# Optimization experiments

Measured on AMD Instinct MI355X. Metric: run time of the kernel, lower is better.

## Reference

```python
import jax, jax.numpy as jnp
import numpy as np

V, D, M, C, L = 100000, 256, 4096, 4096, 32
PAD = 0
EPS = 1e-8  # torch CosineSimilarity default eps


def setup_inputs() -> dict:
    key = jax.random.key(0)
    ks = jax.random.split(key, 6)
    xs = jax.random.randint(ks[0], (1, L), 0, V)
    mems = jax.random.randint(ks[1], (M, L), 0, V)
    ys = jax.random.randint(ks[2], (1, L), 0, V)
    cands = jax.random.randint(ks[3], (C, L), 0, V)
    lt = jax.random.normal(ks[4], (V, D), dtype=jnp.float32) * 0.02
    lt = lt.at[PAD].set(0.0)  # nn.Embedding padding_idx row is zero
    freqs = jax.random.uniform(ks[5], (V,), dtype=jnp.float32, minval=0.05, maxval=1.0)
    return {"xs": xs, "mems": mems, "ys": ys, "cands": cands, "lt": lt, "freqs": freqs}


def _encode(tokens, lt, freqs):
    # Batched Encoder.forward: freq-weighted average of token embeddings.
    # tokens: [N, L] -> [N, D]
    emb = lt[tokens]                       # [N, L, D] gather
    w = freqs[tokens]                      # [N, L]
    w = w / jnp.linalg.norm(w, axis=1, keepdims=True)  # w * (1 / ||w||)
    return jnp.einsum('nl,nld->nd', w, emb)


def reference(xs, mems, ys, cands, lt, freqs):
    xs_emb = _encode(xs, lt, freqs)                                   # [1, D]
    mems_enc = jnp.concatenate([_encode(mems, lt, freqs), xs_emb], 0)  # [M+1, D]
    # cosine similarity of xs_emb (broadcast) against each memory row
    an = jnp.maximum(jnp.linalg.norm(xs_emb, axis=1), EPS)            # [1]
    bn = jnp.maximum(jnp.linalg.norm(mems_enc, axis=1), EPS)          # [M+1]
    cos = (mems_enc @ xs_emb[0]) / (an * bn)                          # [M+1]
    att = jax.nn.softmax(cos)[None, :]                                # [1, M+1]
    lhs_emb = att @ mems_enc                                          # [1, D]
    ys_emb = _encode(ys, lt, freqs)                                   # [1, D]
    cand_emb = _encode(cands, lt, freqs)                              # [C, D]
    # torch.cat of lhs_emb repeated (1 + C) times; ys then cand encodings
    xs_out = jnp.tile(lhs_emb, (cands.shape[0] + 1, 1))               # [C+1, D]
    ys_out = jnp.concatenate([ys_emb, cand_emb], axis=0)              # [C+1, D]
    return xs_out, ys_out
```

## Files before the change

kernel.cpp:

```cpp
#include <hip/hip_runtime.h>

#define V_ 100000
#define D_ 256
#define M_ 4096
#define C_ 4096
#define L_ 32
#define ROWS_MEMS (M_ + 1)
#define NTASK (1 + M_ + 1 + C_)

__device__ __forceinline__ float wave_allreduce_sum(float v) {
    #pragma unroll
    for (int off = 32; off >= 1; off >>= 1) v += __shfl_xor(v, off, 64);
    return v;
}

__device__ __forceinline__ float lane_bcast_f(float v, int l) {
    return __uint_as_float((unsigned)__builtin_amdgcn_readlane((int)__float_as_uint(v), l));
}

__device__ __forceinline__ float4 encode_row(const int* __restrict__ tok_ptr,
                                             const char* __restrict__ ltb,
                                             const float* __restrict__ freqs,
                                             const int lane, const unsigned voff) {
    int tok = 0; float w = 0.f;
    if (lane < L_) { tok = tok_ptr[lane]; w = freqs[tok]; }
    const float s2 = wave_allreduce_sum(w * w);
    const float wn = w / sqrtf(s2);

    float4 acc = make_float4(0.f, 0.f, 0.f, 0.f);
    #pragma unroll
    for (int lb = 0; lb < L_; lb += 8) {
        float4 v[8];
        #pragma unroll
        for (int j = 0; j < 8; ++j) {
            const unsigned t = (unsigned)__builtin_amdgcn_readlane(tok, lb + j);
            v[j] = *reinterpret_cast<const float4*>(
                ltb + t * (unsigned)(D_ * sizeof(float)) + voff);
        }
        #pragma unroll
        for (int j = 0; j < 8; ++j) {
            const float wl = lane_bcast_f(wn, lb + j);
            acc.x = fmaf(wl, v[j].x, acc.x);
            acc.y = fmaf(wl, v[j].y, acc.y);
            acc.z = fmaf(wl, v[j].z, acc.z);
            acc.w = fmaf(wl, v[j].w, acc.w);
        }
    }
    return acc;
}

__global__ __launch_bounds__(256) void encode_fused(
    const int* __restrict__ xs, const int* __restrict__ mems,
    const int* __restrict__ ys, const int* __restrict__ cands,
    const float* __restrict__ lt, const float* __restrict__ freqs,
    float* __restrict__ lhs_raw,
    float* __restrict__ gsum,
    float* __restrict__ out_ys)
{
    __shared__ float s_xf[D_];
    __shared__ float s_an2;
    __shared__ float s_lred[D_];
    __shared__ float s_ered;

    const int wave = threadIdx.x >> 6;
    const int lane = threadIdx.x & 63;
    const int d0 = lane * 4;
    const unsigned voff = (unsigned)d0 * sizeof(float);
    const char* ltb = (const char*)lt;
    const int rt0 = blockIdx.x * 4;
    const bool block_has_att = (rt0 <= M_);

    s_lred[threadIdx.x] = 0.f;
    if (threadIdx.x == 0) s_ered = 0.f;

    if (block_has_att && wave == 0) {
        const float4 xf = encode_row(xs, ltb, freqs, lane, voff);
        *reinterpret_cast<float4*>(&s_xf[d0]) = xf;
        const float an2 = wave_allreduce_sum(xf.x*xf.x + xf.y*xf.y + xf.z*xf.z + xf.w*xf.w);
        if (lane == 0) s_an2 = an2;
    }
    __syncthreads();

    const int rt = rt0 + wave;
    if (rt < NTASK) {
        const int* tok_ptr; float* dst = nullptr; bool has_att = false;
        if (rt == 0) {
            tok_ptr = xs; has_att = true;
        } else if (rt <= M_) {
            tok_ptr = mems + (size_t)(rt - 1) * L_; has_att = true;
        } else if (rt == M_ + 1) {
            tok_ptr = ys; dst = out_ys;
        } else {
            const int c = rt - (M_ + 2);
            tok_ptr = cands + (size_t)c * L_;
            dst = out_ys + (size_t)(c + 1) * D_;
        }

        const float4 acc = encode_row(tok_ptr, ltb, freqs, lane, voff);

        if (has_att) {
            const float4 xf = *reinterpret_cast<const float4*>(&s_xf[d0]);
            const float d = wave_allreduce_sum(acc.x*xf.x + acc.y*xf.y + acc.z*xf.z + acc.w*xf.w);
            const float q = wave_allreduce_sum(acc.x*acc.x + acc.y*acc.y + acc.z*acc.z + acc.w*acc.w);
            const float an = fmaxf(sqrtf(s_an2), 1e-8f);
            const float bn = fmaxf(sqrtf(q),  1e-8f);
            const float e = expf(d / (an * bn));
            atomicAdd(&s_lred[d0 + 0], e * acc.x);
            atomicAdd(&s_lred[d0 + 1], e * acc.y);
            atomicAdd(&s_lred[d0 + 2], e * acc.z);
            atomicAdd(&s_lred[d0 + 3], e * acc.w);
            if (lane == 0) atomicAdd(&s_ered, e);
        } else {
            *reinterpret_cast<float4*>(dst + d0) = acc;
        }
    }

    if (block_has_att) {
        __syncthreads();
        atomicAdd(&lhs_raw[threadIdx.x], s_lred[threadIdx.x]);
        if (threadIdx.x == 0) atomicAdd(gsum, s_ered);
    }
}

__global__ __launch_bounds__(256) void finalize_tile(
    const float* __restrict__ lhs_raw, const float* __restrict__ gsum,
    float* __restrict__ out_xs)
{
    const float val = lhs_raw[threadIdx.x] / gsum[0];
    for (int r = blockIdx.x; r < ROWS_MEMS; r += gridDim.x)
        out_xs[(size_t)r * D_ + threadIdx.x] = val;
}

extern "C" void kernel_launch(void* const* d_in, const int* in_sizes, int n_in,
                              void* d_out, int out_size, void* d_ws, size_t ws_size,
                              hipStream_t stream) {
    const int*   xs    = (const int*)d_in[0];
    const int*   mems  = (const int*)d_in[1];
    const int*   ys    = (const int*)d_in[2];
    const int*   cands = (const int*)d_in[3];
    const float* lt    = (const float*)d_in[4];
    const float* freqs = (const float*)d_in[5];

    float* out    = (float*)d_out;
    float* out_xs = out;
    float* out_ys = out + (size_t)ROWS_MEMS * D_;

    float* lhs_raw = (float*)d_ws;
    float* gsum    = lhs_raw + D_;

    hipMemsetAsync(lhs_raw, 0, (D_ + 1) * sizeof(float), stream);

    encode_fused<<<(NTASK + 3) / 4, 256, 0, stream>>>(xs, mems, ys, cands, lt, freqs,
                                                      lhs_raw, gsum, out_ys);
    finalize_tile<<<1024, 256, 0, stream>>>(lhs_raw, gsum, out_xs);
}
```

Before: 192.1 us.

## Precompute xs encoding in separate kernel and spread atomics over partial buffers

Adds a one-block pre-kernel that encodes xs once and zeroes a set of 32 partial-sum buffers, replacing the memset. Each attention block then loads the precomputed xs vector instead of re-encoding it with a wave. The global atomic accumulation is spread across 32 buffers by block index to reduce contention, and the finalize kernel sums those partials. This costs an extra kernel launch and more reads in finalize.

```diff
diff --git a/kernel.cpp b/kernel.cpp
--- a/kernel.cpp
+++ b/kernel.cpp
@@ -7,6 +7,9 @@
 #define L_ 32
 #define ROWS_MEMS (M_ + 1)
 #define NTASK (1 + M_ + 1 + C_)
+
+#define NBUF 32
+#define BSTRIDE 260
 
 __device__ __forceinline__ float wave_allreduce_sum(float v) {
     #pragma unroll
@@ -18,10 +21,10 @@
     return __uint_as_float((unsigned)__builtin_amdgcn_readlane((int)__float_as_uint(v), l));
 }
 
-__device__ __forceinline__ float4 encode_row(const int* __restrict__ tok_ptr,
-                                             const char* __restrict__ ltb,
-                                             const float* __restrict__ freqs,
-                                             const int lane, const unsigned voff) {
+__device__ __forceinline__ float4 encode_row_f(const int* __restrict__ tok_ptr,
+                                               const char* __restrict__ ltb,
+                                               const float* __restrict__ freqs,
+                                               const int lane, const unsigned voff) {
     int tok = 0; float w = 0.f;
     if (lane < L_) { tok = tok_ptr[lane]; w = freqs[tok]; }
     const float s2 = wave_allreduce_sum(w * w);
@@ -34,8 +37,7 @@
         #pragma unroll
         for (int j = 0; j < 8; ++j) {
             const unsigned t = (unsigned)__builtin_amdgcn_readlane(tok, lb + j);
-            v[j] = *reinterpret_cast<const float4*>(
-                ltb + t * (unsigned)(D_ * sizeof(float)) + voff);
+            v[j] = *reinterpret_cast<const float4*>(ltb + t * 1024u + voff);
         }
         #pragma unroll
         for (int j = 0; j < 8; ++j) {
@@ -49,35 +51,51 @@
     return acc;
 }
 
+__global__ __launch_bounds__(256) void xs_pre(
+    const int* __restrict__ xs, const float* __restrict__ lt,
+    const float* __restrict__ freqs, float* __restrict__ part,
+    float* __restrict__ g_xs)
+{
+    for (int i = threadIdx.x; i < NBUF * BSTRIDE; i += 256) part[i] = 0.f;
+
+    if (threadIdx.x < 64) {
+        const int lane = threadIdx.x;
+        const unsigned voff = (unsigned)lane * 16u;
+        const float4 acc = encode_row_f(xs, (const char*)lt, freqs, lane, voff);
+        *reinterpret_cast<float4*>(g_xs + lane * 4) = acc;
+        const float an2 = wave_allreduce_sum(acc.x*acc.x + acc.y*acc.y +
+                                             acc.z*acc.z + acc.w*acc.w);
+        if (lane == 0) g_xs[256] = an2;
+    }
+}
+
 __global__ __launch_bounds__(256) void encode_fused(
     const int* __restrict__ xs, const int* __restrict__ mems,
     const int* __restrict__ ys, const int* __restrict__ cands,
     const float* __restrict__ lt, const float* __restrict__ freqs,
-    float* __restrict__ lhs_raw,
-    float* __restrict__ gsum,
+    const float* __restrict__ g_xs,
+    float* __restrict__ part,
     float* __restrict__ out_ys)
 {
     __shared__ float s_xf[D_];
-    __shared__ float s_an2;
     __shared__ float s_lred[D_];
     __shared__ float s_ered;
+    __shared__ float s_an2;
 
-    const int wave = threadIdx.x >> 6;
-    const int lane = threadIdx.x & 63;
+    const int tid  = threadIdx.x;
+    const int wave = tid >> 6;
+    const int lane = tid & 63;
     const int d0 = lane * 4;
-    const unsigned voff = (unsigned)d0 * sizeof(float);
+    const unsigned voff = (unsigned)d0 * 4u;
     const char* ltb = (const char*)lt;
     const int rt0 = blockIdx.x * 4;
     const bool block_has_att = (rt0 <= M_);
 
-    s_lred[threadIdx.x] = 0.f;
-    if (threadIdx.x == 0) s_ered = 0.f;
-
-    if (block_has_att && wave == 0) {
-        const float4 xf = encode_row(xs, ltb, freqs, lane, voff);
-        *reinterpret_cast<float4*>(&s_xf[d0]) = xf;
-        const float an2 = wave_allreduce_sum(xf.x*xf.x + xf.y*xf.y + xf.z*xf.z + xf.w*xf.w);
-        if (lane == 0) s_an2 = an2;
+    s_lred[tid] = 0.f;
+    if (tid == 0) s_ered = 0.f;
+    if (block_has_att) {
+        s_xf[tid] = g_xs[tid];
+        if (tid == 0) s_an2 = g_xs[256];
     }
     __syncthreads();
 
@@ -96,7 +114,7 @@
             dst = out_ys + (size_t)(c + 1) * D_;
         }
 
-        const float4 acc = encode_row(tok_ptr, ltb, freqs, lane, voff);
+        const float4 acc = encode_row_f(tok_ptr, ltb, freqs, lane, voff);
 
         if (has_att) {
             const float4 xf = *reinterpret_cast<const float4*>(&s_xf[d0]);
@@ -117,16 +135,22 @@
 
     if (block_has_att) {
         __syncthreads();
-        atomicAdd(&lhs_raw[threadIdx.x], s_lred[threadIdx.x]);
-        if (threadIdx.x == 0) atomicAdd(gsum, s_ered);
+        float* pb = part + (size_t)(blockIdx.x & (NBUF - 1)) * BSTRIDE;
+        atomicAdd(&pb[tid], s_lred[tid]);
+        if (tid == 0) atomicAdd(&pb[256], s_ered);
     }
 }
 
 __global__ __launch_bounds__(256) void finalize_tile(
-    const float* __restrict__ lhs_raw, const float* __restrict__ gsum,
-    float* __restrict__ out_xs)
+    const float* __restrict__ part, float* __restrict__ out_xs)
 {
-    const float val = lhs_raw[threadIdx.x] / gsum[0];
+    float v = 0.f, g = 0.f;
+    #pragma unroll
+    for (int b = 0; b < NBUF; ++b) {
+        v += part[b * BSTRIDE + threadIdx.x];
+        g += part[b * BSTRIDE + 256];
+    }
+    const float val = v / g;
     for (int r = blockIdx.x; r < ROWS_MEMS; r += gridDim.x)
         out_xs[(size_t)r * D_ + threadIdx.x] = val;
 }
@@ -145,12 +169,11 @@
     float* out_xs = out;
     float* out_ys = out + (size_t)ROWS_MEMS * D_;
 
-    float* lhs_raw = (float*)d_ws;
-    float* gsum    = lhs_raw + D_;
+    float* part = (float*)d_ws;
+    float* g_xs = part + NBUF * BSTRIDE;
 
-    hipMemsetAsync(lhs_raw, 0, (D_ + 1) * sizeof(float), stream);
-
-    encode_fused<<<(NTASK + 3) / 4, 256, 0, stream>>>(xs, mems, ys, cands, lt, freqs,
-                                                      lhs_raw, gsum, out_ys);
-    finalize_tile<<<1024, 256, 0, stream>>>(lhs_raw, gsum, out_xs);
+    xs_pre<<<1, 256, 0, stream>>>(xs, lt, freqs, part, g_xs);
+    encode_fused<<<(NTASK + 3) / 4, 256, 0, stream>>>(
+        xs, mems, ys, cands, lt, freqs, g_xs, part, out_ys);
+    finalize_tile<<<1024, 256, 0, stream>>>(part, out_xs);
 }
```

After: 182.1 us, median of 2. -5.2%, faster.
